# Optimization experiments

Hardware: AMD Instinct MI355X
Metric: run time of the kernel (lower is better)

The kernel has to match this reference:

```python
import jax, jax.numpy as jnp
import numpy as np

S = 7          # grid size (7x7)
NUM_CLS = 20   # classes, channels 10:30


def _xyxy(box, m, n):
    # box: [B,4,H,W] with channels (x,y,w,h); faithful to source: x uses row idx m, y uses col idx n
    cx = (box[:, 0] + m) / S
    cy = (box[:, 1] + n) / S
    w, h = box[:, 2], box[:, 3]
    return cx - w / 2, cy - h / 2, cx + w / 2, cy + h / 2


def _iou(b1, b2):
    ix1 = jnp.maximum(b1[0], b2[0])
    iy1 = jnp.maximum(b1[1], b2[1])
    ix2 = jnp.minimum(b1[2], b2[2])
    iy2 = jnp.minimum(b1[3], b2[3])
    inter = jnp.clip(ix2 - ix1, 0.0) * jnp.clip(iy2 - iy1, 0.0)
    a1 = (b1[2] - b1[0]) * (b1[3] - b1[1])
    a2 = (b2[2] - b2[0]) * (b2[3] - b2[1])
    denom = a1 + a2 - inter
    pos = inter > 0
    return jnp.where(pos, inter / jnp.where(pos, denom, 1.0), 0.0)


def setup_inputs() -> dict:
    key = jax.random.key(0)
    k1, k2, k3 = jax.random.split(key, 3)
    B = 16384
    pred = jax.random.uniform(k1, (B, 30, S, S), dtype=jnp.float32) * 0.98 + 0.01
    lab = jax.random.uniform(k2, (B, 30, S, S), dtype=jnp.float32) * 0.9 + 0.05
    conf = (jax.random.uniform(k3, (B, S, S)) < 0.3).astype(jnp.float32)  # obj indicator, exactly 0/1
    lab = lab.at[:, 4].set(conf).at[:, 9].set(conf)
    lab = lab.at[:, 5:9].set(lab[:, 0:4])  # dataset duplicates the gt box for both predictors
    return {"pred": pred, "labels": lab}


def reference(pred, labels):
    B = labels.shape[0]
    m = jnp.arange(S, dtype=pred.dtype).reshape(S, 1)  # row index, broadcast over H axis
    n = jnp.arange(S, dtype=pred.dtype).reshape(1, S)  # col index, broadcast over W axis

    obj = (labels[:, 4] == 1).astype(pred.dtype)       # [B,H,W]
    noobj = 1.0 - obj

    b1 = _xyxy(pred[:, 0:4], m, n)
    b2 = _xyxy(pred[:, 5:9], m, n)
    gt = _xyxy(labels[:, 0:4], m, n)
    iou1 = _iou(b1, gt)
    iou2 = _iou(b2, gt)
    resp1 = (iou1 >= iou2).astype(pred.dtype)          # box1 responsible

    coor1 = 5.0 * (jnp.sum((pred[:, 0:2] - labels[:, 0:2]) ** 2, axis=1)
                   + jnp.sum((jnp.sqrt(pred[:, 2:4]) - jnp.sqrt(labels[:, 2:4])) ** 2, axis=1))
    coor2 = 5.0 * (jnp.sum((pred[:, 5:7] - labels[:, 5:7]) ** 2, axis=1)
                   + jnp.sum((jnp.sqrt(pred[:, 7:9]) - jnp.sqrt(labels[:, 7:9])) ** 2, axis=1))

    objc1 = (pred[:, 4] - iou1) ** 2
    objc2 = (pred[:, 9] - iou2) ** 2

    coor = resp1 * coor1 + (1 - resp1) * coor2
    obj_conf = resp1 * objc1 + (1 - resp1) * objc2
    noobj_resp = 0.5 * (resp1 * objc2 + (1 - resp1) * objc1)  # non-responsible box in obj cell
    cls = jnp.sum((pred[:, 10:] - labels[:, 10:]) ** 2, axis=1)

    noobj_cell = 0.5 * (pred[:, 4] ** 2 + pred[:, 9] ** 2)    # cells with no object

    loss = jnp.sum(obj * (coor + obj_conf + noobj_resp + cls)) + jnp.sum(noobj * noobj_cell)
    return loss / B
```

## Files before the change

### kernel.cpp

```cpp
#include <hip/hip_runtime.h>

#define S7 7
#define NCELL 49
#define CH 30
#define IMG_F (CH * NCELL)
#define K_IMG 2
#define BLK 256
#define NF4 (K_IMG * IMG_F / 4)

typedef __attribute__((address_space(1))) const void global_cvoid;
typedef __attribute__((address_space(3))) void lds_void;

__global__ __launch_bounds__(BLK) void yolo_loss_stage1(
    const float4* __restrict__ pred4,
    const float4* __restrict__ lab4,
    float* __restrict__ partials,
    int B)
{
    __shared__ float4 sp4[NF4];
    __shared__ float4 sl4[NF4];
    const float* sp = (const float*)sp4;
    const float* sl = (const float*)sl4;

    const size_t g4base = (size_t)blockIdx.x * NF4;
    const size_t total4 = ((size_t)B * IMG_F) / 4;
    for (int i = threadIdx.x; i < NF4; i += BLK) {
        if (g4base + i < total4) {
            __builtin_amdgcn_global_load_lds(
                (global_cvoid*)(pred4 + g4base + i),
                (lds_void*)(&sp4[i]), 16, 0, 0);
            __builtin_amdgcn_global_load_lds(
                (global_cvoid*)(lab4 + g4base + i),
                (lds_void*)(&sl4[i]), 16, 0, 0);
        }
    }
    __syncthreads();

    const int b0 = blockIdx.x * K_IMG;
    const int nimg = (B - b0 < K_IMG) ? (B - b0) : K_IMG;

    float contrib = 0.0f;
    const int tid = threadIdx.x;
    if (tid < nimg * NCELL) {
        const int img  = tid / NCELL;
        const int cell = tid - img * NCELL;
        const float* __restrict__ pb = sp + img * IMG_F + cell;
        const float* __restrict__ lb = sl + img * IMG_F + cell;

        float p[10], l[10];
        #pragma unroll
        for (int c = 0; c < 10; ++c) {
            p[c] = pb[c * NCELL];
            l[c] = lb[c * NCELL];
        }
        float cls = 0.0f;
        #pragma unroll
        for (int c = 10; c < CH; ++c) {
            float d = pb[c * NCELL] - lb[c * NCELL];
            cls += d * d;
        }

        const int   row = cell / S7;
        const float mi = (float)row;
        const float nj = (float)(cell - row * S7);
        const float invS = 1.0f / 7.0f;

        float ax1, ay1, ax2, ay2;
        {
            float cx = (p[0] + mi) * invS, cy = (p[1] + nj) * invS;
            ax1 = cx - 0.5f * p[2]; ay1 = cy - 0.5f * p[3];
            ax2 = cx + 0.5f * p[2]; ay2 = cy + 0.5f * p[3];
        }
        float bx1, by1, bx2, by2;
        {
            float cx = (p[5] + mi) * invS, cy = (p[6] + nj) * invS;
            bx1 = cx - 0.5f * p[7]; by1 = cy - 0.5f * p[8];
            bx2 = cx + 0.5f * p[7]; by2 = cy + 0.5f * p[8];
        }
        float gx1, gy1, gx2, gy2;
        {
            float cx = (l[0] + mi) * invS, cy = (l[1] + nj) * invS;
            gx1 = cx - 0.5f * l[2]; gy1 = cy - 0.5f * l[3];
            gx2 = cx + 0.5f * l[2]; gy2 = cy + 0.5f * l[3];
        }

        float iou1, iou2;
        {
            float ix1 = fmaxf(ax1, gx1), iy1 = fmaxf(ay1, gy1);
            float ix2 = fminf(ax2, gx2), iy2 = fminf(ay2, gy2);
            float inter = fmaxf(ix2 - ix1, 0.0f) * fmaxf(iy2 - iy1, 0.0f);
            float a1 = (ax2 - ax1) * (ay2 - ay1);
            float a2 = (gx2 - gx1) * (gy2 - gy1);
            float denom = a1 + a2 - inter;
            iou1 = (inter > 0.0f) ? inter / denom : 0.0f;
        }
        {
            float ix1 = fmaxf(bx1, gx1), iy1 = fmaxf(by1, gy1);
            float ix2 = fminf(bx2, gx2), iy2 = fminf(by2, gy2);
            float inter = fmaxf(ix2 - ix1, 0.0f) * fmaxf(iy2 - iy1, 0.0f);
            float a1 = (bx2 - bx1) * (by2 - by1);
            float a2 = (gx2 - gx1) * (gy2 - gy1);
            float denom = a1 + a2 - inter;
            iou2 = (inter > 0.0f) ? inter / denom : 0.0f;
        }

        const bool resp1 = (iou1 >= iou2);

        float d0 = p[0] - l[0], d1 = p[1] - l[1];
        float s2 = __builtin_sqrtf(p[2]) - __builtin_sqrtf(l[2]);
        float s3 = __builtin_sqrtf(p[3]) - __builtin_sqrtf(l[3]);
        float coor1 = 5.0f * (d0 * d0 + d1 * d1 + s2 * s2 + s3 * s3);

        float e0 = p[5] - l[5], e1 = p[6] - l[6];
        float t2 = __builtin_sqrtf(p[7]) - __builtin_sqrtf(l[7]);
        float t3 = __builtin_sqrtf(p[8]) - __builtin_sqrtf(l[8]);
        float coor2 = 5.0f * (e0 * e0 + e1 * e1 + t2 * t2 + t3 * t3);

        float o1 = p[4] - iou1; o1 *= o1;
        float o2 = p[9] - iou2; o2 *= o2;

        float coor       = resp1 ? coor1 : coor2;
        float obj_conf   = resp1 ? o1 : o2;
        float noobj_resp = 0.5f * (resp1 ? o2 : o1);
        float noobj_cell = 0.5f * (p[4] * p[4] + p[9] * p[9]);

        const bool obj = (l[4] == 1.0f);
        contrib = obj ? (coor + obj_conf + noobj_resp + cls) : noobj_cell;
    }

    #pragma unroll
    for (int off = 32; off > 0; off >>= 1)
        contrib += __shfl_down(contrib, off, 64);

    __shared__ float wsum[BLK / 64];
    const int lane = threadIdx.x & 63;
    const int wid  = threadIdx.x >> 6;
    if (lane == 0) wsum[wid] = contrib;
    __syncthreads();
    if (threadIdx.x == 0)
        partials[blockIdx.x] = wsum[0] + wsum[1] + wsum[2] + wsum[3];
}

__global__ __launch_bounds__(1024) void yolo_loss_stage2(
    const float* __restrict__ partials,
    float* __restrict__ out,
    int nparts, float inv_B)
{
    float s = 0.0f;
    for (int i = threadIdx.x; i < nparts; i += 1024)
        s += partials[i];

    #pragma unroll
    for (int off = 32; off > 0; off >>= 1)
        s += __shfl_down(s, off, 64);

    __shared__ float wsum[16];
    const int lane = threadIdx.x & 63;
    const int wid  = threadIdx.x >> 6;
    if (lane == 0) wsum[wid] = s;
    __syncthreads();
    if (threadIdx.x == 0) {
        float bs = 0.0f;
        #pragma unroll
        for (int w = 0; w < 16; ++w) bs += wsum[w];
        out[0] = bs * inv_B;
    }
}

extern "C" void kernel_launch(void* const* d_in, const int* in_sizes, int n_in,
                              void* d_out, int out_size, void* d_ws, size_t ws_size,
                              hipStream_t stream) {
    const float4* pred4 = (const float4*)d_in[0];
    const float4* lab4  = (const float4*)d_in[1];
    float* out = (float*)d_out;
    float* partials = (float*)d_ws;

    const int B = in_sizes[0] / IMG_F;
    const int grid = (B + K_IMG - 1) / K_IMG;

    yolo_loss_stage1<<<grid, BLK, 0, stream>>>(pred4, lab4, partials, B);
    yolo_loss_stage2<<<1, 1024, 0, stream>>>(partials, out, grid, 1.0f / (float)B);
}
```

Measured before the change: 36.79 us.

## Switch stage1 to persistent grid-stride blocks with 512 threads

```diff
diff --git a/kernel.cpp b/kernel.cpp
--- a/kernel.cpp
+++ b/kernel.cpp
@@ -5,8 +5,9 @@
 #define CH 30
 #define IMG_F (CH * NCELL)
 #define K_IMG 2
-#define BLK 256
+#define BLK 512
 #define NF4 (K_IMG * IMG_F / 4)
+#define GRID 1024
 
 typedef __attribute__((address_space(1))) const void global_cvoid;
 typedef __attribute__((address_space(3))) void lds_void;
@@ -15,17 +16,19 @@
     const float4* __restrict__ pred4,
     const float4* __restrict__ lab4,
     float* __restrict__ partials,
-    int B)
+    int npairs)
 {
     __shared__ float4 sp4[NF4];
     __shared__ float4 sl4[NF4];
     const float* sp = (const float*)sp4;
     const float* sl = (const float*)sl4;
 
-    const size_t g4base = (size_t)blockIdx.x * NF4;
-    const size_t total4 = ((size_t)B * IMG_F) / 4;
-    for (int i = threadIdx.x; i < NF4; i += BLK) {
-        if (g4base + i < total4) {
+    const int tid = threadIdx.x;
+    float contrib = 0.0f;
+
+    for (int pair = blockIdx.x; pair < npairs; pair += gridDim.x) {
+        const size_t g4base = (size_t)pair * NF4;
+        for (int i = tid; i < NF4; i += BLK) {
             __builtin_amdgcn_global_load_lds(
                 (global_cvoid*)(pred4 + g4base + i),
                 (lds_void*)(&sp4[i]), 16, 0, 0);
@@ -33,99 +36,95 @@
                 (global_cvoid*)(lab4 + g4base + i),
                 (lds_void*)(&sl4[i]), 16, 0, 0);
         }
-    }
-    __syncthreads();
+        __syncthreads();
 
-    const int b0 = blockIdx.x * K_IMG;
-    const int nimg = (B - b0 < K_IMG) ? (B - b0) : K_IMG;
+        if (tid < K_IMG * NCELL) {
+            const int img  = tid / NCELL;
+            const int cell = tid - img * NCELL;
+            const float* __restrict__ pb = sp + img * IMG_F + cell;
+            const float* __restrict__ lb = sl + img * IMG_F + cell;
 
-    float contrib = 0.0f;
-    const int tid = threadIdx.x;
-    if (tid < nimg * NCELL) {
-        const int img  = tid / NCELL;
-        const int cell = tid - img * NCELL;
-        const float* __restrict__ pb = sp + img * IMG_F + cell;
-        const float* __restrict__ lb = sl + img * IMG_F + cell;
+            float p[10], l[10];
+            #pragma unroll
+            for (int c = 0; c < 10; ++c) {
+                p[c] = pb[c * NCELL];
+                l[c] = lb[c * NCELL];
+            }
+            float cls = 0.0f;
+            #pragma unroll
+            for (int c = 10; c < CH; ++c) {
+                float d = pb[c * NCELL] - lb[c * NCELL];
+                cls += d * d;
+            }
 
-        float p[10], l[10];
-        #pragma unroll
-        for (int c = 0; c < 10; ++c) {
-            p[c] = pb[c * NCELL];
-            l[c] = lb[c * NCELL];
+            const int   row = cell / S7;
+            const float mi = (float)row;
+            const float nj = (float)(cell - row * S7);
+            const float invS = 1.0f / 7.0f;
+
+            float ax1, ay1, ax2, ay2;
+            {
+                float cx = (p[0] + mi) * invS, cy = (p[1] + nj) * invS;
+                ax1 = cx - 0.5f * p[2]; ay1 = cy - 0.5f * p[3];
+                ax2 = cx + 0.5f * p[2]; ay2 = cy + 0.5f * p[3];
+            }
+            float bx1, by1, bx2, by2;
+            {
+                float cx = (p[5] + mi) * invS, cy = (p[6] + nj) * invS;
+                bx1 = cx - 0.5f * p[7]; by1 = cy - 0.5f * p[8];
+                bx2 = cx + 0.5f * p[7]; by2 = cy + 0.5f * p[8];
+            }
+            float gx1, gy1, gx2, gy2;
+            {
+                float cx = (l[0] + mi) * invS, cy = (l[1] + nj) * invS;
+                gx1 = cx - 0.5f * l[2]; gy1 = cy - 0.5f * l[3];
+                gx2 = cx + 0.5f * l[2]; gy2 = cy + 0.5f * l[3];
+            }
+
+            float iou1, iou2;
+            {
+                float ix1 = fmaxf(ax1, gx1), iy1 = fmaxf(ay1, gy1);
+                float ix2 = fminf(ax2, gx2), iy2 = fminf(ay2, gy2);
+                float inter = fmaxf(ix2 - ix1, 0.0f) * fmaxf(iy2 - iy1, 0.0f);
+                float a1 = (ax2 - ax1) * (ay2 - ay1);
+                float a2 = (gx2 - gx1) * (gy2 - gy1);
+                float denom = a1 + a2 - inter;
+                iou1 = (inter > 0.0f) ? inter / denom : 0.0f;
+            }
+            {
+                float ix1 = fmaxf(bx1, gx1), iy1 = fmaxf(by1, gy1);
+                float ix2 = fminf(bx2, gx2), iy2 = fminf(by2, gy2);
+                float inter = fmaxf(ix2 - ix1, 0.0f) * fmaxf(iy2 - iy1, 0.0f);
+                float a1 = (bx2 - bx1) * (by2 - by1);
+                float a2 = (gx2 - gx1) * (gy2 - gy1);
+                float denom = a1 + a2 - inter;
+                iou2 = (inter > 0.0f) ? inter / denom : 0.0f;
+            }
+
+            const bool resp1 = (iou1 >= iou2);
+
+            float d0 = p[0] - l[0], d1 = p[1] - l[1];
+            float s2 = __builtin_sqrtf(p[2]) - __builtin_sqrtf(l[2]);
+            float s3 = __builtin_sqrtf(p[3]) - __builtin_sqrtf(l[3]);
+            float coor1 = 5.0f * (d0 * d0 + d1 * d1 + s2 * s2 + s3 * s3);
+
+            float e0 = p[5] - l[5], e1 = p[6] - l[6];
+            float t2 = __builtin_sqrtf(p[7]) - __builtin_sqrtf(l[7]);
+            float t3 = __builtin_sqrtf(p[8]) - __builtin_sqrtf(l[8]);
+            float coor2 = 5.0f * (e0 * e0 + e1 * e1 + t2 * t2 + t3 * t3);
+
+            float o1 = p[4] - iou1; o1 *= o1;
+            float o2 = p[9] - iou2; o2 *= o2;
+
+            float coor       = resp1 ? coor1 : coor2;
+            float obj_conf   = resp1 ? o1 : o2;
+            float noobj_resp = 0.5f * (resp1 ? o2 : o1);
+            float noobj_cell = 0.5f * (p[4] * p[4] + p[9] * p[9]);
+
+            const bool obj = (l[4] == 1.0f);
+            contrib += obj ? (coor + obj_conf + noobj_resp + cls) : noobj_cell;
         }
-        float cls = 0.0f;
-        #pragma unroll
-        for (int c = 10; c < CH; ++c) {
-            float d = pb[c * NCELL] - lb[c * NCELL];
-            cls += d * d;
-        }
-
-        const int   row = cell / S7;
-        const float mi = (float)row;
-        const float nj = (float)(cell - row * S7);
-        const float invS = 1.0f / 7.0f;
-
-        float ax1, ay1, ax2, ay2;
-        {
-            float cx = (p[0] + mi) * invS, cy = (p[1] + nj) * invS;
-            ax1 = cx - 0.5f * p[2]; ay1 = cy - 0.5f * p[3];
-            ax2 = cx + 0.5f * p[2]; ay2 = cy + 0.5f * p[3];
-        }
-        float bx1, by1, bx2, by2;
-        {
-            float cx = (p[5] + mi) * invS, cy = (p[6] + nj) * invS;
-            bx1 = cx - 0.5f * p[7]; by1 = cy - 0.5f * p[8];
-            bx2 = cx + 0.5f * p[7]; by2 = cy + 0.5f * p[8];
-        }
-        float gx1, gy1, gx2, gy2;
-        {
-            float cx = (l[0] + mi) * invS, cy = (l[1] + nj) * invS;
-            gx1 = cx - 0.5f * l[2]; gy1 = cy - 0.5f * l[3];
-            gx2 = cx + 0.5f * l[2]; gy2 = cy + 0.5f * l[3];
-        }
-
-        float iou1, iou2;
-        {
-            float ix1 = fmaxf(ax1, gx1), iy1 = fmaxf(ay1, gy1);
-            float ix2 = fminf(ax2, gx2), iy2 = fminf(ay2, gy2);
-            float inter = fmaxf(ix2 - ix1, 0.0f) * fmaxf(iy2 - iy1, 0.0f);
-            float a1 = (ax2 - ax1) * (ay2 - ay1);
-            float a2 = (gx2 - gx1) * (gy2 - gy1);
-            float denom = a1 + a2 - inter;
-            iou1 = (inter > 0.0f) ? inter / denom : 0.0f;
-        }
-        {
-            float ix1 = fmaxf(bx1, gx1), iy1 = fmaxf(by1, gy1);
-            float ix2 = fminf(bx2, gx2), iy2 = fminf(by2, gy2);
-            float inter = fmaxf(ix2 - ix1, 0.0f) * fmaxf(iy2 - iy1, 0.0f);
-            float a1 = (bx2 - bx1) * (by2 - by1);
-            float a2 = (gx2 - gx1) * (gy2 - gy1);
-            float denom = a1 + a2 - inter;
-            iou2 = (inter > 0.0f) ? inter / denom : 0.0f;
-        }
-
-        const bool resp1 = (iou1 >= iou2);
-
-        float d0 = p[0] - l[0], d1 = p[1] - l[1];
-        float s2 = __builtin_sqrtf(p[2]) - __builtin_sqrtf(l[2]);
-        float s3 = __builtin_sqrtf(p[3]) - __builtin_sqrtf(l[3]);
-        float coor1 = 5.0f * (d0 * d0 + d1 * d1 + s2 * s2 + s3 * s3);
-
-        float e0 = p[5] - l[5], e1 = p[6] - l[6];
-        float t2 = __builtin_sqrtf(p[7]) - __builtin_sqrtf(l[7]);
-        float t3 = __builtin_sqrtf(p[8]) - __builtin_sqrtf(l[8]);
-        float coor2 = 5.0f * (e0 * e0 + e1 * e1 + t2 * t2 + t3 * t3);
-
-        float o1 = p[4] - iou1; o1 *= o1;
-        float o2 = p[9] - iou2; o2 *= o2;
-
-        float coor       = resp1 ? coor1 : coor2;
-        float obj_conf   = resp1 ? o1 : o2;
-        float noobj_resp = 0.5f * (resp1 ? o2 : o1);
-        float noobj_cell = 0.5f * (p[4] * p[4] + p[9] * p[9]);
-
-        const bool obj = (l[4] == 1.0f);
-        contrib = obj ? (coor + obj_conf + noobj_resp + cls) : noobj_cell;
+        __syncthreads();
     }
 
     #pragma unroll
@@ -133,12 +132,16 @@
         contrib += __shfl_down(contrib, off, 64);
 
     __shared__ float wsum[BLK / 64];
-    const int lane = threadIdx.x & 63;
-    const int wid  = threadIdx.x >> 6;
+    const int lane = tid & 63;
+    const int wid  = tid >> 6;
     if (lane == 0) wsum[wid] = contrib;
     __syncthreads();
-    if (threadIdx.x == 0)
-        partials[blockIdx.x] = wsum[0] + wsum[1] + wsum[2] + wsum[3];
+    if (tid == 0) {
+        float bs = 0.0f;
+        #pragma unroll
+        for (int w = 0; w < BLK / 64; ++w) bs += wsum[w];
+        partials[blockIdx.x] = bs;
+    }
 }
 
 __global__ __launch_bounds__(1024) void yolo_loss_stage2(
@@ -146,9 +149,7 @@
     float* __restrict__ out,
     int nparts, float inv_B)
 {
-    float s = 0.0f;
-    for (int i = threadIdx.x; i < nparts; i += 1024)
-        s += partials[i];
+    float s = (threadIdx.x < nparts) ? partials[threadIdx.x] : 0.0f;
 
     #pragma unroll
     for (int off = 32; off > 0; off >>= 1)
@@ -176,8 +177,9 @@
     float* partials = (float*)d_ws;
 
     const int B = in_sizes[0] / IMG_F;
-    const int grid = (B + K_IMG - 1) / K_IMG;
+    const int npairs = B / K_IMG;
+    const int grid = (npairs < GRID) ? npairs : GRID;
 
-    yolo_loss_stage1<<<grid, BLK, 0, stream>>>(pred4, lab4, partials, B);
+    yolo_loss_stage1<<<grid, BLK, 0, stream>>>(pred4, lab4, partials, npairs);
     yolo_loss_stage2<<<1, 1024, 0, stream>>>(partials, out, grid, 1.0f / (float)B);
 }
```

Result: no change. 37.29 us (+1.4%).
